# Performance work log

Hardware: AMD Instinct MI355X
Metric: run time of the kernel (lower is better)

The kernel has to match this reference:

```python
import jax, jax.numpy as jnp
import numpy as np

D = 128          # embedding dim
N_INIT = 100000  # number of initial (axiom) clauses
L = 64           # topological levels of derived clauses
M = 4096         # derived clauses per level
N_THAX = 2000    # distinct axiom-name (thax) embeddings
N_SINE = 32      # sine-level embeddings
N_RULES = 256    # distinct inference rules (each with its own 2-ary MLP)
N_TOT = N_INIT + L * M


def setup_inputs() -> dict:
    key = jax.random.key(0)
    ks = jax.random.split(key, 10)
    rng = np.random.default_rng(0)
    # parents of level-l nodes point to any node created strictly earlier
    parents = np.stack(
        [rng.integers(0, N_INIT + l * M, size=(M, 2)) for l in range(L)]
    ).astype(np.int32)  # [L, M, 2]
    return {
        "thax_table": jax.random.normal(ks[0], (N_THAX, D), jnp.float32) * 0.1,
        "sine_table": jax.random.normal(ks[1], (N_SINE, D), jnp.float32) * 0.1,
        "rule_W": jax.random.normal(ks[2], (N_RULES, 2 * D, D), jnp.float32) * (1.0 / np.sqrt(2 * D)),
        "rule_b": jax.random.normal(ks[3], (N_RULES, D), jnp.float32) * 0.01,
        "eval_w": jax.random.normal(ks[4], (D,), jnp.float32) * (1.0 / np.sqrt(D)),
        "eval_b": jax.random.normal(ks[5], (1,), jnp.float32) * 0.01,
        "pos_vals": jax.random.uniform(ks[6], (N_TOT,), jnp.float32, 0.01, 1.0),
        "neg_vals": jax.random.uniform(ks[7], (N_TOT,), jnp.float32, 0.01, 1.0),
        "init_thax": jax.random.randint(ks[8], (N_INIT,), 0, N_THAX, jnp.int32),
        "init_sine": jax.random.randint(ks[9], (N_INIT,), 0, N_SINE, jnp.int32),
        "parents": jnp.asarray(parents),
        "rules": jnp.asarray(rng.integers(0, N_RULES, size=(L, M)).astype(np.int32)),
    }


def reference(thax_table, sine_table, rule_W, rule_b, eval_w, eval_b,
              pos_vals, neg_vals, init_thax, init_sine, parents, rules):
    n_init = init_thax.shape[0]
    n_lvl, m = rules.shape
    d = thax_table.shape[1]

    # init nodes: embed = init_embeds[thax]() + sine_embedder(sine)
    init_emb = thax_table[init_thax] + sine_table[init_sine]  # [N_INIT, D]
    store0 = jnp.concatenate(
        [init_emb, jnp.zeros((n_lvl * m, d), init_emb.dtype)], axis=0)  # [N_TOT, D]

    # deriv nodes, level by level: gather 2 parents, per-rule MLP (cat -> Linear -> ReLU)
    def step(store, xs):
        lvl, par, rul = xs                       # par: [M,2] int, rul: [M] int
        pe = store[par].reshape(m, 2 * d)        # gather parent embeddings
        emb = jax.nn.relu(jnp.einsum('mi,mio->mo', pe, rule_W[rul]) + rule_b[rul])
        store = jax.lax.dynamic_update_slice(store, emb, (n_init + lvl * m, 0))
        return store, None

    store, _ = jax.lax.scan(step, store0, (jnp.arange(n_lvl), parents, rules))

    # eval_net + weighted BCEWithLogits (pos_weight = tot_neg / tot_pos)
    logits = store @ eval_w + eval_b[0]          # [N_TOT]
    tot = pos_vals + neg_vals
    y = pos_vals / tot
    pw = jnp.sum(neg_vals) / jnp.sum(pos_vals)
    per_node = pw * y * jax.nn.softplus(-logits) + (1.0 - y) * jax.nn.softplus(logits)
    loss = jnp.sum(tot * per_node).reshape(1)
    posOK = jnp.sum(jnp.where(logits >= 0.0, pos_vals, 0.0))
    negOK = jnp.sum(jnp.where(logits < 0.0, neg_vals, 0.0))
    return (loss, posOK, negOK)
```

## Files before the change

kernel.cpp:

```cpp
#include <hip/hip_runtime.h>

#define D      128
#define NINIT  100000
#define LVLS   64
#define M      4096
#define NRULES 256
#define NTOT   (NINIT + LVLS * M)
#define NTHR   512
#define TILE   32

typedef __attribute__((ext_vector_type(8))) short short8;
typedef __attribute__((ext_vector_type(4))) float floatx4;

#define ST_OFF 256
#define SI_OFF (ST_OFF + (size_t)NTOT * D * 2)
#define RO_OFF (SI_OFF + (size_t)LVLS * M * 4)
#define FL_OFF (RO_OFF + (size_t)LVLS * (NRULES + 1) * 4)

#define CBAR() asm volatile("" ::: "memory")

__device__ __forceinline__ unsigned short f2bf(float x) {
  unsigned u = __float_as_uint(x);
  u += 0x7fffu + ((u >> 16) & 1u);
  return (unsigned short)(u >> 16);
}

__device__ __forceinline__ float softplusf(float x) {
  return fmaxf(x, 0.f) + log1pf(expf(-fabsf(x)));
}

__device__ __forceinline__ void st_sys(unsigned* p, unsigned v) {
  __hip_atomic_store(p, v, __ATOMIC_RELAXED, __HIP_MEMORY_SCOPE_SYSTEM);
}
__device__ __forceinline__ void st_sys64(unsigned long long* p,
                                         unsigned long long v) {
  __hip_atomic_store(p, v, __ATOMIC_RELAXED, __HIP_MEMORY_SCOPE_SYSTEM);
}
__device__ __forceinline__ unsigned ld_sys(const unsigned* p) {
  return __hip_atomic_load(p, __ATOMIC_RELAXED, __HIP_MEMORY_SCOPE_SYSTEM);
}
__device__ __forceinline__ void wait_flag(const unsigned* f) {
  int guard = 1 << 17;
  while (__builtin_expect(ld_sys(f) == 0u, 0) && --guard)
    __builtin_amdgcn_s_sleep(1);
  CBAR();
}

__device__ __forceinline__ void gbar_light(unsigned* bcnt, unsigned* bgen) {
  __syncthreads();
  if (threadIdx.x == 0) {
    unsigned g = ld_sys(bgen);
    unsigned v = __hip_atomic_fetch_add(bcnt, 1u, __ATOMIC_RELAXED,
                                        __HIP_MEMORY_SCOPE_SYSTEM);
    if (v == gridDim.x - 1) {
      st_sys(bcnt, 0u);
      st_sys(bgen, g + 1u);
    } else {
      int guard = 1 << 22;
      while (ld_sys(bgen) == g && --guard) __builtin_amdgcn_s_sleep(2);
    }
  }
  __syncthreads();
}

__device__ __forceinline__ bool adv_cursor(int r, const int* __restrict__ ro,
                                           int& l, int& t0, int& off, int& cnt) {
  t0 += TILE;
  while (t0 >= cnt) {
    if (++l >= LVLS) return false;
    off = ro[l * (NRULES + 1) + r];
    cnt = ro[l * (NRULES + 1) + r + 1] - off;
    t0 = 0;
  }
  return true;
}

__global__ __launch_bounds__(NTHR, 2) void fused_kernel(
    const float* __restrict__ thax_table, const float* __restrict__ sine_table,
    const float* __restrict__ rule_W, const float* __restrict__ rule_b,
    const float* __restrict__ eval_w, const float* __restrict__ eval_b,
    const float* __restrict__ pos, const float* __restrict__ neg,
    const int* __restrict__ init_thax, const int* __restrict__ init_sine,
    const int* __restrict__ parents,
    const int* __restrict__ rules,
    unsigned short* __restrict__ store, int* __restrict__ sorted_idx,
    int* __restrict__ rule_off, unsigned* __restrict__ flags,
    float* __restrict__ sums, unsigned* __restrict__ bvars,
    float* __restrict__ out) {
  __shared__ unsigned short pe[TILE * 264];
  __shared__ unsigned short ot[TILE * 136];
  __shared__ int s_sid[2][TILE];
  __shared__ int s_cnt[NRULES];
  __shared__ int s_base[NRULES + 1];
  __shared__ float racc[3];

  unsigned* bcnt = bvars;
  unsigned* bgen = bvars + 1;

  const int r = blockIdx.x;
  const int tid = threadIdx.x;
  const int wave = tid >> 6, lane = tid & 63;
  const int col = (wave << 4) + (lane & 15);
  const int node = tid >> 4;
  const int segq = tid & 15;
  const int gid = r * NTHR + tid;
  const int gthreads = NRULES * NTHR;

  float a_loss = 0.f, a_pos = 0.f, a_neg = 0.f;
  const float eb = eval_b[0];
  float w8[8];
  {
    float4 wA = ((const float4*)eval_w)[segq * 2];
    float4 wB = ((const float4*)eval_w)[segq * 2 + 1];
    w8[0] = wA.x; w8[1] = wA.y; w8[2] = wA.z; w8[3] = wA.w;
    w8[4] = wB.x; w8[5] = wB.y; w8[6] = wB.z; w8[7] = wB.w;
  }

  short8 bf[8];
  {
    const float* Wr = rule_W + (size_t)r * (2 * D * D);
    const int krow_base = (lane >> 4) * 8;
#pragma unroll
    for (int ks = 0; ks < 8; ++ks) {
      union { short8 s; unsigned short us[8]; } c;
#pragma unroll
      for (int j = 0; j < 8; ++j)
        c.us[j] = f2bf(Wr[(size_t)(ks * 32 + krow_base + j) * D + col]);
      bf[ks] = c.s;
    }
  }
  const float bias = rule_b[r * D + col];

  if (r < LVLS) {
    const int l = r;
    const int* rl = rules + (size_t)l * M;
    if (tid < NRULES) s_cnt[tid] = 0;
    __syncthreads();
    for (int m = tid; m < M; m += NTHR) atomicAdd(&s_cnt[rl[m]], 1);
    __syncthreads();
    if (tid == 0) {
      int run = 0;
      for (int q = 0; q < NRULES; ++q) { s_base[q] = run; run += s_cnt[q]; }
      s_base[NRULES] = run;
    }
    __syncthreads();
    if (tid < NRULES) {
      st_sys((unsigned*)&rule_off[(size_t)l * (NRULES + 1) + tid],
             (unsigned)s_base[tid]);
      s_cnt[tid] = s_base[tid];
    }
    if (tid == 0)
      st_sys((unsigned*)&rule_off[(size_t)l * (NRULES + 1) + NRULES],
             (unsigned)M);
    __syncthreads();
    for (int m = tid; m < M; m += NTHR) {
      int p = atomicAdd(&s_cnt[rl[m]], 1);
      st_sys((unsigned*)&sorted_idx[(size_t)l * M + p], (unsigned)m);
    }
  }

  for (int idx = gid; idx < NINIT * 16; idx += gthreads) {
    int nd = idx >> 4, sg = idx & 15;
    const float4* t = (const float4*)(thax_table + (size_t)init_thax[nd] * D) + sg * 2;
    const float4* s = (const float4*)(sine_table + (size_t)init_sine[nd] * D) + sg * 2;
    float4 a0 = t[0], a1 = t[1], b0 = s[0], b1 = s[1];
    float v[8] = {a0.x + b0.x, a0.y + b0.y, a0.z + b0.z, a0.w + b0.w,
                  a1.x + b1.x, a1.y + b1.y, a1.z + b1.z, a1.w + b1.w};
    unsigned p0 = (unsigned)f2bf(v[0]) | ((unsigned)f2bf(v[1]) << 16);
    unsigned p1 = (unsigned)f2bf(v[2]) | ((unsigned)f2bf(v[3]) << 16);
    unsigned p2 = (unsigned)f2bf(v[4]) | ((unsigned)f2bf(v[5]) << 16);
    unsigned p3 = (unsigned)f2bf(v[6]) | ((unsigned)f2bf(v[7]) << 16);
    unsigned long long* dst =
        (unsigned long long*)(store + (size_t)nd * D + sg * 8);
    st_sys64(dst + 0, (unsigned long long)p0 | ((unsigned long long)p1 << 32));
    st_sys64(dst + 1, (unsigned long long)p2 | ((unsigned long long)p3 << 32));
  }

  {
    float sp = 0.f, sn = 0.f;
    for (int i = gid; i < NTOT; i += gthreads) {
      sp += pos[i];
      sn += neg[i];
    }
    for (int m = 32; m; m >>= 1) {
      sp += __shfl_xor(sp, m, 64);
      sn += __shfl_xor(sn, m, 64);
    }
    if (lane == 0) {
      atomicAdd(&sums[0], sp);
      atomicAdd(&sums[1], sn);
    }
  }

  gbar_light(bcnt, bgen);

  const float pw = sums[1] / sums[0];

  int lL = -1, t0L = 0, offL = 0, cntL = 0;

  bool validA = adv_cursor(r, rule_off, lL, t0L, offL, cntL);
  int lA = lL, t0A = t0L, cntA = cntL;
  int parA0 = 0, parA1 = 0;
  bool lateA0 = false, lateA1 = false;
  unsigned reA0 = 1u, reA1 = 1u;
  float pPosA = 0.f, pNegA = 0.f;
  uint4 gA0 = {0, 0, 0, 0}, gA1 = {0, 0, 0, 0};
  if (validA) {
    int gj = t0A + node; if (gj > cntA - 1) gj = cntA - 1;
    int sid = sorted_idx[(size_t)lA * M + offL + gj];
    parA0 = parents[((size_t)lA * M + sid) * 2 + 0];
    parA1 = parents[((size_t)lA * M + sid) * 2 + 1];
    pPosA = pos[NINIT + lA * M + sid];
    pNegA = neg[NINIT + lA * M + sid];
    if (parA0 >= NINIT) wait_flag(flags + (parA0 - NINIT));
    if (parA1 >= NINIT) wait_flag(flags + (parA1 - NINIT));
    gA0 = *(const uint4*)(store + (size_t)parA0 * D + segq * 8);
    gA1 = *(const uint4*)(store + (size_t)parA1 * D + segq * 8);
    if (segq == 0) s_sid[0][node] = sid;
  }

  bool validB = validA && adv_cursor(r, rule_off, lL, t0L, offL, cntL);
  int lB = lL, t0B = t0L, cntB = cntL;
  int sidB = 0, parB0 = 0, parB1 = 0;
  unsigned fB0 = 1u, fB1 = 1u;
  if (validB) {
    int gj = t0B + node; if (gj > cntB - 1) gj = cntB - 1;
    sidB = sorted_idx[(size_t)lB * M + offL + gj];
    parB0 = parents[((size_t)lB * M + sidB) * 2 + 0];
    parB1 = parents[((size_t)lB * M + sidB) * 2 + 1];
    fB0 = parB0 >= NINIT ? ld_sys(flags + (parB0 - NINIT)) : 1u;
    fB1 = parB1 >= NINIT ? ld_sys(flags + (parB1 - NINIT)) : 1u;
  }

  bool validC = validB && adv_cursor(r, rule_off, lL, t0L, offL, cntL);
  int lC = lL, t0C = t0L, cntC = cntL;
  int sidC = 0, parC0 = 0, parC1 = 0;
  if (validC) {
    int gj = t0C + node; if (gj > cntC - 1) gj = cntC - 1;
    sidC = sorted_idx[(size_t)lC * M + offL + gj];
    parC0 = parents[((size_t)lC * M + sidC) * 2 + 0];
    parC1 = parents[((size_t)lC * M + sidC) * 2 + 1];
  }

  bool validD = validC && adv_cursor(r, rule_off, lL, t0L, offL, cntL);
  int lD = lL, t0D = t0L, offD = offL, cntD = cntL;

  int p = 0;
  while (validA) {
    if (lateA0 || lateA1) {
      bool n0 = lateA0 && (reA0 == 0u);
      bool n1 = lateA1 && (reA1 == 0u);
      if (n0 || n1) {
        int guard = 1 << 17;
        while (guard--) {
          unsigned f0 = n0 ? ld_sys(flags + (parA0 - NINIT)) : 1u;
          unsigned f1 = n1 ? ld_sys(flags + (parA1 - NINIT)) : 1u;
          if (f0 != 0u && f1 != 0u) break;
          __builtin_amdgcn_s_sleep(1);
        }
      }
      CBAR();
      if (lateA0) gA0 = *(const uint4*)(store + (size_t)parA0 * D + segq * 8);
      if (lateA1) gA1 = *(const uint4*)(store + (size_t)parA1 * D + segq * 8);
    }

    *(uint4*)(pe + node * 264 + segq * 8) = gA0;
    *(uint4*)(pe + node * 264 + 128 + segq * 8) = gA1;
    __syncthreads();
    if (validB && segq == 0) s_sid[p ^ 1][node] = sidB;

    floatx4 acc0 = {0.f, 0.f, 0.f, 0.f}, acc1 = {0.f, 0.f, 0.f, 0.f};
#pragma unroll
    for (int ks = 0; ks < 8; ++ks) {
      short8 a0 = *(const short8*)(pe + (lane & 15) * 264 + ks * 32 + (lane >> 4) * 8);
      short8 a1 = *(const short8*)(pe + (16 + (lane & 15)) * 264 + ks * 32 + (lane >> 4) * 8);
      acc0 = __builtin_amdgcn_mfma_f32_16x16x32_bf16(a0, bf[ks], acc0, 0, 0, 0);
      acc1 = __builtin_amdgcn_mfma_f32_16x16x32_bf16(a1, bf[ks], acc1, 0, 0, 0);
    }
#pragma unroll
    for (int reg = 0; reg < 4; ++reg) {
      int row = (lane >> 4) * 4 + reg;
      float v0 = acc0[reg] + bias;
      float v1 = acc1[reg] + bias;
      ot[row * 136 + col] = f2bf(v0 > 0.f ? v0 : 0.f);
      ot[(16 + row) * 136 + col] = f2bf(v1 > 0.f ? v1 : 0.f);
    }
    __syncthreads();

    {
      const int n_baseA = NINIT + lA * M;
      int nsid[4]; bool inr[4]; int S = 0;
#pragma unroll
      for (int k = 0; k < 4; ++k) {
        int nd = wave + 8 * k;
        nsid[k] = s_sid[p][nd];
        inr[k] = (t0A + nd) < cntA;
        if (inr[k]) {
          st_sys((unsigned*)(store + (size_t)(n_baseA + nsid[k]) * D) + lane,
                 *(const unsigned*)(ot + nd * 136 + lane * 2));
          ++S;
        }
      }
      CBAR();
#pragma unroll
      for (int k = 0; k < 4; ++k) {
        if (inr[k]) {
          if (S == 4)      asm volatile("s_waitcnt vmcnt(3)" ::: "memory");
          else if (S == 3) asm volatile("s_waitcnt vmcnt(2)" ::: "memory");
          else if (S == 2) asm volatile("s_waitcnt vmcnt(1)" ::: "memory");
          else             asm volatile("s_waitcnt vmcnt(0)" ::: "memory");
          if (lane == 0) st_sys(flags + lA * M + nsid[k], 1u);
        }
      }
      CBAR();
    }

    bool lateB0 = validB && parB0 >= NINIT && fB0 == 0u;
    bool lateB1 = validB && parB1 >= NINIT && fB1 == 0u;
    uint4 gB0, gB1;
    {
      const unsigned short* a0 =
          (validB && !lateB0) ? store + (size_t)parB0 * D : store;
      const unsigned short* a1 =
          (validB && !lateB1) ? store + (size_t)parB1 * D : store;
      gB0 = *(const uint4*)(a0 + segq * 8);
      gB1 = *(const uint4*)(a1 + segq * 8);
    }
    float pPosB = 0.f, pNegB = 0.f;
    if (validB) {
      pPosB = pos[NINIT + lB * M + sidB];
      pNegB = neg[NINIT + lB * M + sidB];
    }
    int sidD = 0, parD0 = 0, parD1 = 0;
    if (validD) {
      int gj = t0D + node; if (gj > cntD - 1) gj = cntD - 1;
      sidD = sorted_idx[(size_t)lD * M + offD + gj];
      parD0 = parents[((size_t)lD * M + sidD) * 2 + 0];
      parD1 = parents[((size_t)lD * M + sidD) * 2 + 1];
    }
    unsigned fC0 = 1u, fC1 = 1u;
    if (validC) {
      fC0 = ld_sys(flags + (parC0 >= NINIT ? parC0 - NINIT : 0));
      fC1 = ld_sys(flags + (parC1 >= NINIT ? parC1 - NINIT : 0));
      if (parC0 < NINIT) fC0 = 1u;
      if (parC1 < NINIT) fC1 = 1u;
    }
    unsigned reB0 = 1u, reB1 = 1u;
    if (lateB0) reB0 = ld_sys(flags + (parB0 - NINIT));
    if (lateB1) reB1 = ld_sys(flags + (parB1 - NINIT));
    CBAR();

    {
      const uint4 u = *(const uint4*)(ot + node * 136 + segq * 8);
      float pd = __uint_as_float(u.x << 16) * w8[0] +
                 __uint_as_float(u.x & 0xffff0000u) * w8[1] +
                 __uint_as_float(u.y << 16) * w8[2] +
                 __uint_as_float(u.y & 0xffff0000u) * w8[3] +
                 __uint_as_float(u.z << 16) * w8[4] +
                 __uint_as_float(u.z & 0xffff0000u) * w8[5] +
                 __uint_as_float(u.w << 16) * w8[6] +
                 __uint_as_float(u.w & 0xffff0000u) * w8[7];
      pd += __shfl_xor(pd, 1, 64);
      pd += __shfl_xor(pd, 2, 64);
      pd += __shfl_xor(pd, 4, 64);
      pd += __shfl_xor(pd, 8, 64);
      if (segq == 0 && (t0A + node) < cntA) {
        float logit = pd + eb;
        float tot = pPosA + pNegA, y = pPosA / tot;
        a_loss += tot * (pw * y * softplusf(-logit) +
                         (1.f - y) * softplusf(logit));
        if (logit >= 0.f) a_pos += pPosA; else a_neg += pNegA;
      }
    }

    gA0 = gB0; gA1 = gB1; lateA0 = lateB0; lateA1 = lateB1;
    reA0 = reB0; reA1 = reB1;
    parA0 = parB0; parA1 = parB1;
    pPosA = pPosB; pNegA = pNegB;
    lA = lB; t0A = t0B; cntA = cntB; validA = validB;
    sidB = sidC; parB0 = parC0; parB1 = parC1; fB0 = fC0; fB1 = fC1;
    lB = lC; t0B = t0C; cntB = cntC; validB = validC;
    sidC = sidD; parC0 = parD0; parC1 = parD1;
    lC = lD; t0C = t0D; cntC = cntD; validC = validD;
    validD = validC && adv_cursor(r, rule_off, lL, t0L, offL, cntL);
    lD = lL; t0D = t0L; offD = offL; cntD = cntL;
    p ^= 1;
  }

  {
    const float4* wv = (const float4*)eval_w;
    for (int nd = gid; nd < NINIT; nd += gthreads) {
      const uint4* v = (const uint4*)(store + (size_t)nd * D);
      float dot = 0.f;
#pragma unroll
      for (int k = 0; k < 16; ++k) {
        uint4 u = v[k];
        float4 w0 = wv[k * 2], w1 = wv[k * 2 + 1];
        dot += __uint_as_float(u.x << 16) * w0.x +
               __uint_as_float(u.x & 0xffff0000u) * w0.y +
               __uint_as_float(u.y << 16) * w0.z +
               __uint_as_float(u.y & 0xffff0000u) * w0.w +
               __uint_as_float(u.z << 16) * w1.x +
               __uint_as_float(u.z & 0xffff0000u) * w1.y +
               __uint_as_float(u.w << 16) * w1.z +
               __uint_as_float(u.w & 0xffff0000u) * w1.w;
      }
      float logit = dot + eb;
      float pp = pos[nd], nn = neg[nd];
      float tot = pp + nn, y = pp / tot;
      a_loss += tot * (pw * y * softplusf(-logit) + (1.f - y) * softplusf(logit));
      if (logit >= 0.f) a_pos += pp; else a_neg += nn;
    }
  }

  for (int m = 32; m; m >>= 1) {
    a_loss += __shfl_xor(a_loss, m, 64);
    a_pos  += __shfl_xor(a_pos,  m, 64);
    a_neg  += __shfl_xor(a_neg,  m, 64);
  }
  if (tid == 0) { racc[0] = 0.f; racc[1] = 0.f; racc[2] = 0.f; }
  __syncthreads();
  if (lane == 0) {
    atomicAdd(&racc[0], a_loss);
    atomicAdd(&racc[1], a_pos);
    atomicAdd(&racc[2], a_neg);
  }
  __syncthreads();
  if (tid == 0) {
    atomicAdd(&out[0], racc[0]);
    atomicAdd(&out[1], racc[1]);
    atomicAdd(&out[2], racc[2]);
  }
}

extern "C" void kernel_launch(void* const* d_in, const int* in_sizes, int n_in,
                              void* d_out, int out_size, void* d_ws, size_t ws_size,
                              hipStream_t stream) {
  const float* thax_table = (const float*)d_in[0];
  const float* sine_table = (const float*)d_in[1];
  const float* rule_W     = (const float*)d_in[2];
  const float* rule_b     = (const float*)d_in[3];
  const float* eval_w     = (const float*)d_in[4];
  const float* eval_b     = (const float*)d_in[5];
  const float* pos_vals   = (const float*)d_in[6];
  const float* neg_vals   = (const float*)d_in[7];
  const int*   init_thax  = (const int*)d_in[8];
  const int*   init_sine  = (const int*)d_in[9];
  const int*   parents    = (const int*)d_in[10];
  const int*   rules      = (const int*)d_in[11];

  float* out = (float*)d_out;
  char* ws = (char*)d_ws;
  float* sums = (float*)ws;
  unsigned* bvars = (unsigned*)(ws + 128);
  unsigned short* store = (unsigned short*)(ws + ST_OFF);
  int* sorted_idx = (int*)(ws + SI_OFF);
  int* rule_off   = (int*)(ws + RO_OFF);
  unsigned* flags = (unsigned*)(ws + FL_OFF);

  (void)hipMemsetAsync(d_out, 0, 3 * sizeof(float), stream);
  (void)hipMemsetAsync(d_ws, 0, 256, stream);
  (void)hipMemsetAsync(ws + FL_OFF, 0, (size_t)LVLS * M * 4, stream);

  void* args[] = {&thax_table, &sine_table, &rule_W, &rule_b, &eval_w, &eval_b,
                  &pos_vals, &neg_vals, &init_thax, &init_sine, &parents,
                  &rules, &store, &sorted_idx, &rule_off, &flags, &sums,
                  &bvars, &out};
  (void)hipLaunchCooperativeKernel((void*)fused_kernel, dim3(NRULES),
                                   dim3(NTHR), args, 0, stream);
}
```

Before: 418.5 us.

## Fuse init-node loss into embedding pass and defer pos_weight factor

The loss for initial nodes is now computed while their embeddings are built, using the fp32 values and a shuffle-reduced dot product. This removes the trailing pass that re-read the bf16 store for all init nodes. The positive and negative loss terms are accumulated separately so that pos_weight can be applied once at the end, since pw is not yet known when the init pass runs. The init logits now come from unrounded fp32 rather than bf16, which shifts numerics slightly.

```diff
diff --git a/kernel.cpp b/kernel.cpp
--- a/kernel.cpp
+++ b/kernel.cpp
@@ -92,7 +92,7 @@
   __shared__ int s_sid[2][TILE];
   __shared__ int s_cnt[NRULES];
   __shared__ int s_base[NRULES + 1];
-  __shared__ float racc[3];
+  __shared__ float racc[4];
 
   unsigned* bcnt = bvars;
   unsigned* bgen = bvars + 1;
@@ -106,7 +106,7 @@
   const int gid = r * NTHR + tid;
   const int gthreads = NRULES * NTHR;
 
-  float a_loss = 0.f, a_pos = 0.f, a_neg = 0.f;
+  float aP1 = 0.f, aP2 = 0.f, a_pos = 0.f, a_neg = 0.f;
   const float eb = eval_b[0];
   float w8[8];
   {
@@ -174,6 +174,21 @@
         (unsigned long long*)(store + (size_t)nd * D + sg * 8);
     st_sys64(dst + 0, (unsigned long long)p0 | ((unsigned long long)p1 << 32));
     st_sys64(dst + 1, (unsigned long long)p2 | ((unsigned long long)p3 << 32));
+
+    float pd = v[0] * w8[0] + v[1] * w8[1] + v[2] * w8[2] + v[3] * w8[3] +
+               v[4] * w8[4] + v[5] * w8[5] + v[6] * w8[6] + v[7] * w8[7];
+    pd += __shfl_xor(pd, 1, 64);
+    pd += __shfl_xor(pd, 2, 64);
+    pd += __shfl_xor(pd, 4, 64);
+    pd += __shfl_xor(pd, 8, 64);
+    if (sg == 0) {
+      float logit = pd + eb;
+      float pp = pos[nd], nn = neg[nd];
+      float tot = pp + nn, y = pp / tot;
+      aP1 += tot * y * softplusf(-logit);
+      aP2 += tot * (1.f - y) * softplusf(logit);
+      if (logit >= 0.f) a_pos += pp; else a_neg += nn;
+    }
   }
 
   {
@@ -367,8 +382,8 @@
       if (segq == 0 && (t0A + node) < cntA) {
         float logit = pd + eb;
         float tot = pPosA + pNegA, y = pPosA / tot;
-        a_loss += tot * (pw * y * softplusf(-logit) +
-                         (1.f - y) * softplusf(logit));
+        aP1 += tot * y * softplusf(-logit);
+        aP2 += tot * (1.f - y) * softplusf(logit);
         if (logit >= 0.f) a_pos += pPosA; else a_neg += pNegA;
       }
     }
@@ -387,49 +402,25 @@
     p ^= 1;
   }
 
-  {
-    const float4* wv = (const float4*)eval_w;
-    for (int nd = gid; nd < NINIT; nd += gthreads) {
-      const uint4* v = (const uint4*)(store + (size_t)nd * D);
-      float dot = 0.f;
-#pragma unroll
-      for (int k = 0; k < 16; ++k) {
-        uint4 u = v[k];
-        float4 w0 = wv[k * 2], w1 = wv[k * 2 + 1];
-        dot += __uint_as_float(u.x << 16) * w0.x +
-               __uint_as_float(u.x & 0xffff0000u) * w0.y +
-               __uint_as_float(u.y << 16) * w0.z +
-               __uint_as_float(u.y & 0xffff0000u) * w0.w +
-               __uint_as_float(u.z << 16) * w1.x +
-               __uint_as_float(u.z & 0xffff0000u) * w1.y +
-               __uint_as_float(u.w << 16) * w1.z +
-               __uint_as_float(u.w & 0xffff0000u) * w1.w;
-      }
-      float logit = dot + eb;
-      float pp = pos[nd], nn = neg[nd];
-      float tot = pp + nn, y = pp / tot;
-      a_loss += tot * (pw * y * softplusf(-logit) + (1.f - y) * softplusf(logit));
-      if (logit >= 0.f) a_pos += pp; else a_neg += nn;
-    }
-  }
-
   for (int m = 32; m; m >>= 1) {
-    a_loss += __shfl_xor(a_loss, m, 64);
-    a_pos  += __shfl_xor(a_pos,  m, 64);
-    a_neg  += __shfl_xor(a_neg,  m, 64);
-  }
-  if (tid == 0) { racc[0] = 0.f; racc[1] = 0.f; racc[2] = 0.f; }
+    aP1   += __shfl_xor(aP1,   m, 64);
+    aP2   += __shfl_xor(aP2,   m, 64);
+    a_pos += __shfl_xor(a_pos, m, 64);
+    a_neg += __shfl_xor(a_neg, m, 64);
+  }
+  if (tid == 0) { racc[0] = 0.f; racc[1] = 0.f; racc[2] = 0.f; racc[3] = 0.f; }
   __syncthreads();
   if (lane == 0) {
-    atomicAdd(&racc[0], a_loss);
-    atomicAdd(&racc[1], a_pos);
-    atomicAdd(&racc[2], a_neg);
+    atomicAdd(&racc[0], aP1);
+    atomicAdd(&racc[1], aP2);
+    atomicAdd(&racc[2], a_pos);
+    atomicAdd(&racc[3], a_neg);
   }
   __syncthreads();
   if (tid == 0) {
-    atomicAdd(&out[0], racc[0]);
-    atomicAdd(&out[1], racc[1]);
-    atomicAdd(&out[2], racc[2]);
+    atomicAdd(&out[0], pw * racc[0] + racc[1]);
+    atomicAdd(&out[1], racc[2]);
+    atomicAdd(&out[2], racc[3]);
   }
 }
 
```

After: 419.8 us. No clear change (+0.3%).
